# Kernel optimization log

Measured on AMD Instinct MI355X. Metric: run time of the kernel, lower is better.

The kernel has to match this reference:

```python
import jax, jax.numpy as jnp
import numpy as np

B, N, IN_DIM, DIM, HEADS = 2, 4096, 1024, 1024, 8
MAX_MASK = 2048
SCALE = DIM ** -0.5  # original uses full dim, not per-head dim


def setup_inputs() -> dict:
    key = jax.random.key(0)
    k_x, k_qkv, k_o, k_b, k_m = jax.random.split(key, 5)
    x = jax.random.normal(k_x, (B, N, IN_DIM), dtype=jnp.float32)
    W_qkv = jax.random.normal(k_qkv, (IN_DIM, 3 * DIM), dtype=jnp.float32) * 0.02
    W_out = jax.random.normal(k_o, (DIM, DIM), dtype=jnp.float32) * 0.02
    b_out = jax.random.normal(k_b, (DIM,), dtype=jnp.float32) * 0.02
    mask = jax.random.randint(k_m, (1, 1, MAX_MASK, MAX_MASK), 0, 2, dtype=jnp.int32)
    return {"x": x, "W_qkv": W_qkv, "W_out": W_out, "b_out": b_out,
            "mask": mask, "max_mask": MAX_MASK}


def reference(x, W_qkv, W_out, b_out, mask, max_mask):
    b, n, _ = x.shape
    d = DIM // HEADS
    qkv = x @ W_qkv                                   # [b, n, 3*dim]
    qkv = qkv.reshape(b, n, 3, HEADS, d).transpose(2, 0, 3, 1, 4)  # [3, b, h, n, d]
    q, k, v = qkv[0], qkv[1], qkv[2]
    dots = jnp.einsum('bhid,bhjd->bhij', q, k) * SCALE  # [b, h, n, n]
    # partial submatrix masking on the top-left [max_mask, max_mask] block
    m = max_mask
    sub = jnp.where(mask == 0, -jnp.inf, dots[:, :, :m, :m])
    dots = dots.at[:, :, :m, :m].set(sub)
    attn = jax.nn.softmax(dots, axis=-1)
    out = jnp.einsum('bhij,bhjd->bhid', attn, v)       # [b, h, n, d]
    out = out.transpose(0, 2, 1, 3).reshape(b, n, HEADS * d)
    return out @ W_out + b_out
```

## Files before the change

kernel.cpp:

```cpp
#include <hip/hip_runtime.h>
#include <hip/hip_bf16.h>
#include <stdint.h>


typedef __attribute__((ext_vector_type(8))) short short8;
typedef __attribute__((ext_vector_type(4))) float f32x4;

#define SCALE_Q 0.03125f

__device__ __forceinline__ unsigned short f2bf(float f) {
  union { float f; unsigned int u; } v;
  v.f = f;
  return (unsigned short)((v.u + 0x7fffu + ((v.u >> 16) & 1u)) >> 16);
}

__device__ __forceinline__ unsigned int pkbf2(float a, float b) {
  __hip_bfloat162 h = __float22bfloat162_rn(make_float2(a, b));
  union { __hip_bfloat162 h; unsigned int u; } c;
  c.h = h;
  return c.u;
}

__device__ __forceinline__ void gload_lds16(const void* g, void* l) {
  __builtin_amdgcn_global_load_lds(
      (const __attribute__((address_space(1))) uint32_t*)(uintptr_t)g,
      (__attribute__((address_space(3))) uint32_t*)(uintptr_t)l, 16, 0, 0);
}

__device__ __forceinline__ f32x4 zero4() {
  f32x4 z; z.x = 0.f; z.y = 0.f; z.z = 0.f; z.w = 0.f; return z;
}

__global__ __launch_bounds__(256) void k_cvt_x(const float* __restrict__ in,
                                               unsigned short* __restrict__ out) {
  const int t = blockIdx.x * 256 + threadIdx.x;
  const float4 v = ((const float4*)in)[t];
  ushort4 o;
  o.x = f2bf(v.x); o.y = f2bf(v.y); o.z = f2bf(v.z); o.w = f2bf(v.w);
  ((ushort4*)out)[t] = o;
}

__global__ __launch_bounds__(256) void k_cvt_wt(const float* __restrict__ w,
                                                unsigned short* __restrict__ wt,
                                                int Nn) {
  __shared__ float t[32][33];
  const int n0 = blockIdx.x << 5, k0 = blockIdx.y << 5;
  const int c = threadIdx.x & 31, r8 = threadIdx.x >> 5;
#pragma unroll
  for (int i = 0; i < 4; ++i) {
    const int r = (i << 3) + r8;
    t[r][c] = w[(long)(k0 + r) * Nn + n0 + c];
  }
  __syncthreads();
#pragma unroll
  for (int i = 0; i < 4; ++i) {
    const int r = (i << 3) + r8;
    wt[(long)(n0 + r) * 1024 + k0 + c] = f2bf(t[c][r]);
  }
}

__global__ __launch_bounds__(256, 2) void k_qkv_gemm(
    const unsigned short* __restrict__ A,
    const unsigned short* __restrict__ Bt,
    unsigned short* __restrict__ Qs, unsigned short* __restrict__ Ks,
    unsigned short* __restrict__ Vt) {
  __shared__ __align__(16) unsigned short lA[4][128][8];
  __shared__ __align__(16) unsigned short lB[4][128][8];
  const int tid = threadIdx.x;
  const int w = tid >> 6, ln = tid & 63;
  const int m15 = ln & 15, q4 = ln >> 4;
  const int wm = (w >> 1) << 6, wn = (w & 1) << 6;
  const int tn = blockIdx.x, tm = blockIdx.y;
  const int which = tn >> 3;
  const int h = tn & 7;

  f32x4 acc[4][4];
#pragma unroll
  for (int i = 0; i < 4; ++i)
#pragma unroll
    for (int j = 0; j < 4; ++j) acc[i][j] = zero4();

  if (which == 2) {
    for (int kb = 0; kb < 1024; kb += 32) {
      __syncthreads();
#pragma unroll
      for (int c = 0; c < 2; ++c) {
        const int p = ((c * 4 + w) << 10) + (ln << 4);
        const int g = p >> 11;
        const int r = (p & 2047) >> 4;
        gload_lds16(A + ((long)tm * 128 + r) * 1024 + kb + g * 8,
                    (char*)&lA[0][0][0] + p);
        gload_lds16(Bt + ((long)tn * 128 + r) * 1024 + kb + g * 8,
                    (char*)&lB[0][0][0] + p);
      }
      __syncthreads();
      short8 afr[4], bfr[4];
#pragma unroll
      for (int i = 0; i < 4; ++i)
        afr[i] = *(const short8*)&lA[q4][wm + i * 16 + m15][0];
#pragma unroll
      for (int j = 0; j < 4; ++j)
        bfr[j] = *(const short8*)&lB[q4][wn + j * 16 + m15][0];
#pragma unroll
      for (int i = 0; i < 4; ++i)
#pragma unroll
        for (int j = 0; j < 4; ++j)
          acc[i][j] = __builtin_amdgcn_mfma_f32_16x16x32_bf16(afr[i], bfr[j],
                                                              acc[i][j], 0, 0, 0);
    }
#pragma unroll
    for (int i = 0; i < 4; ++i) {
      const int m0 = (tm << 7) + wm + (i << 4) + (q4 << 2);
      const int b = m0 >> 12, row0 = m0 & 4095;
#pragma unroll
      for (int j = 0; j < 4; ++j) {
        const int dd = wn + (j << 4) + m15;
        const long bh = b * 8 + h;
        uint2 u;
        u.x = pkbf2(acc[i][j][0], acc[i][j][1]);
        u.y = pkbf2(acc[i][j][2], acc[i][j][3]);
        *(uint2*)&Vt[(bh * 128 + dd) * 4096 + row0] = u;
      }
    }
  } else {
    for (int kb = 0; kb < 1024; kb += 32) {
      __syncthreads();
#pragma unroll
      for (int c = 0; c < 2; ++c) {
        const int p = ((c * 4 + w) << 10) + (ln << 4);
        const int g = p >> 11;
        const int r = (p & 2047) >> 4;
        gload_lds16(A + ((long)tm * 128 + r) * 1024 + kb + g * 8,
                    (char*)&lA[0][0][0] + p);
        gload_lds16(Bt + ((long)tn * 128 + r) * 1024 + kb + g * 8,
                    (char*)&lB[0][0][0] + p);
      }
      __syncthreads();
      short8 afr[4], bfr[4];
#pragma unroll
      for (int i = 0; i < 4; ++i)
        afr[i] = *(const short8*)&lA[q4][wm + i * 16 + m15][0];
#pragma unroll
      for (int j = 0; j < 4; ++j)
        bfr[j] = *(const short8*)&lB[q4][wn + j * 16 + m15][0];
#pragma unroll
      for (int i = 0; i < 4; ++i)
#pragma unroll
        for (int j = 0; j < 4; ++j)
          acc[i][j] = __builtin_amdgcn_mfma_f32_16x16x32_bf16(bfr[j], afr[i],
                                                              acc[i][j], 0, 0, 0);
    }
    unsigned short* Dst = (which == 0) ? Qs : Ks;
    const float sc = (which == 0) ? SCALE_Q : 1.0f;
#pragma unroll
    for (int i = 0; i < 4; ++i) {
      const int m = (tm << 7) + wm + (i << 4) + m15;
      const int b = m >> 12, row = m & 4095;
      const long bh = b * 8 + h;
#pragma unroll
      for (int j = 0; j < 4; ++j) {
        const int dd0 = wn + (j << 4) + (q4 << 2);
        uint2 u;
        u.x = pkbf2(acc[i][j][0] * sc, acc[i][j][1] * sc);
        u.y = pkbf2(acc[i][j][2] * sc, acc[i][j][3] * sc);
        *(uint2*)&Dst[(bh * 4096 + row) * 128 + dd0] = u;
      }
    }
  }
}

__global__ __launch_bounds__(512, 2) void k_flash(
    const unsigned short* __restrict__ Qs, const unsigned short* __restrict__ Ks,
    const unsigned short* __restrict__ Vt, const int* __restrict__ mask,
    unsigned short* __restrict__ Ob) {
  __shared__ __align__(16) unsigned short lK[16][64][8];
  __shared__ __align__(16) unsigned short lV[8][128][8];
  __shared__ __align__(16) unsigned short lP[8][16][72];

  const int tid = threadIdx.x;
  const int w = tid >> 6, ln = tid & 63;
  const int m15 = ln & 15, q4 = ln >> 4;
  const int rowblk = blockIdx.x, bh = blockIdx.y;
  const int rbase = rowblk * 128 + w * 16;
  const int qrow = rbase + m15;

  const unsigned short* Qbh = Qs + (long)bh * 524288;
  const unsigned short* Kbh = Ks + (long)bh * 524288;
  const unsigned short* Vbh = Vt + (long)bh * 524288;

  short8 qf[4];
#pragma unroll
  for (int kk = 0; kk < 4; ++kk)
    qf[kk] = *(const short8*)(Qbh + (long)qrow * 128 + kk * 32 + q4 * 8);

  f32x4 o[8];
#pragma unroll
  for (int j = 0; j < 8; ++j) o[j] = zero4();
  f32x4 lacc = zero4();

  const bool maskblk = rowblk < 16;

  for (int kv = 0; kv < 4096; kv += 64) {
    __syncthreads();
#pragma unroll
    for (int c = 0; c < 2; ++c) {
      const int p = ((c * 8 + w) << 10) + (ln << 4);
      const int cs = p >> 10;
      const int j = (p & 1023) >> 4;
      gload_lds16(Kbh + (long)(kv + j) * 128 + cs * 8, (char*)&lK[0][0][0] + p);
    }
#pragma unroll
    for (int c = 0; c < 2; ++c) {
      const int p = ((c * 8 + w) << 10) + (ln << 4);
      const int cv = p >> 11;
      const int dv = (p & 2047) >> 4;
      gload_lds16(Vbh + (long)dv * 4096 + kv + cv * 8, (char*)&lV[0][0][0] + p);
    }
    __syncthreads();

    f32x4 s[4];
#pragma unroll
    for (int jt = 0; jt < 4; ++jt) s[jt] = zero4();
#pragma unroll
    for (int jt = 0; jt < 4; ++jt) {
#pragma unroll
      for (int kk = 0; kk < 4; ++kk) {
        const short8 kfr = *(const short8*)&lK[kk * 4 + q4][jt * 16 + m15][0];
        s[jt] = __builtin_amdgcn_mfma_f32_16x16x32_bf16(kfr, qf[kk], s[jt],
                                                        0, 0, 0);
      }
    }

    if (maskblk && kv < 2048) {
#pragma unroll
      for (int jt = 0; jt < 4; ++jt) {
        const int4 mv =
            *(const int4*)&mask[(long)qrow * 2048 + kv + jt * 16 + q4 * 4];
        s[jt].x = mv.x ? s[jt].x : -1e30f;
        s[jt].y = mv.y ? s[jt].y : -1e30f;
        s[jt].z = mv.z ? s[jt].z : -1e30f;
        s[jt].w = mv.w ? s[jt].w : -1e30f;
      }
    }

#pragma unroll
    for (int jt = 0; jt < 4; ++jt) {
      f32x4 p;
      p.x = __expf(s[jt].x); p.y = __expf(s[jt].y);
      p.z = __expf(s[jt].z); p.w = __expf(s[jt].w);
      lacc.x += p.x; lacc.y += p.y; lacc.z += p.z; lacc.w += p.w;
      uint2 u;
      u.x = pkbf2(p.x, p.y);
      u.y = pkbf2(p.z, p.w);
      *(uint2*)&lP[w][m15][jt * 16 + q4 * 4] = u;
    }
    __asm__ volatile("s_waitcnt lgkmcnt(0)" ::: "memory");

#pragma unroll
    for (int kk2 = 0; kk2 < 2; ++kk2) {
      const short8 pf = *(const short8*)&lP[w][m15][kk2 * 32 + q4 * 8];
#pragma unroll
      for (int jt2 = 0; jt2 < 8; ++jt2) {
        const short8 vf = *(const short8*)&lV[kk2 * 4 + q4][jt2 * 16 + m15][0];
        o[jt2] = __builtin_amdgcn_mfma_f32_16x16x32_bf16(pf, vf, o[jt2],
                                                         0, 0, 0);
      }
    }
  }

  float lh = lacc.x + lacc.y + lacc.z + lacc.w;
  lh += __shfl_xor(lh, 16);
  lh += __shfl_xor(lh, 32);
  const float linv = 1.0f / lh;
  float linv_r[4];
#pragma unroll
  for (int r = 0; r < 4; ++r) linv_r[r] = __shfl(linv, q4 * 4 + r);

  const int b = bh >> 3, h = bh & 7;
#pragma unroll
  for (int r = 0; r < 4; ++r) {
    const int row = rbase + q4 * 4 + r;
    unsigned short* op = Ob + ((long)(b * 4096 + row)) * 1024 + h * 128;
#pragma unroll
    for (int jt2 = 0; jt2 < 8; ++jt2)
      op[jt2 * 16 + m15] = f2bf(o[jt2][r] * linv_r[r]);
  }
}

__global__ __launch_bounds__(256, 2) void k_proj_gemm(
    const unsigned short* __restrict__ A,
    const unsigned short* __restrict__ Bt,
    const float* __restrict__ bias, float* __restrict__ Out) {
  __shared__ __align__(16) unsigned short lA[4][128][8];
  __shared__ __align__(16) unsigned short lB[4][128][8];
  const int tid = threadIdx.x;
  const int w = tid >> 6, ln = tid & 63;
  const int m15 = ln & 15, q4 = ln >> 4;
  const int wm = (w >> 1) << 6, wn = (w & 1) << 6;
  const int tn = blockIdx.x, tm = blockIdx.y;

  f32x4 acc[4][4];
#pragma unroll
  for (int i = 0; i < 4; ++i)
#pragma unroll
    for (int j = 0; j < 4; ++j) acc[i][j] = zero4();

  for (int kb = 0; kb < 1024; kb += 32) {
    __syncthreads();
#pragma unroll
    for (int c = 0; c < 2; ++c) {
      const int p = ((c * 4 + w) << 10) + (ln << 4);
      const int g = p >> 11;
      const int r = (p & 2047) >> 4;
      gload_lds16(A + ((long)tm * 128 + r) * 1024 + kb + g * 8,
                  (char*)&lA[0][0][0] + p);
      gload_lds16(Bt + ((long)tn * 128 + r) * 1024 + kb + g * 8,
                  (char*)&lB[0][0][0] + p);
    }
    __syncthreads();
    short8 afr[4], bfr[4];
#pragma unroll
    for (int i = 0; i < 4; ++i)
      afr[i] = *(const short8*)&lA[q4][wm + i * 16 + m15][0];
#pragma unroll
    for (int j = 0; j < 4; ++j)
      bfr[j] = *(const short8*)&lB[q4][wn + j * 16 + m15][0];
#pragma unroll
    for (int i = 0; i < 4; ++i)
#pragma unroll
      for (int j = 0; j < 4; ++j)
        acc[i][j] = __builtin_amdgcn_mfma_f32_16x16x32_bf16(afr[i], bfr[j],
                                                            acc[i][j], 0, 0, 0);
  }

#pragma unroll
  for (int i = 0; i < 4; ++i)
#pragma unroll
    for (int r = 0; r < 4; ++r) {
      const int m = (tm << 7) + wm + (i << 4) + (q4 << 2) + r;
#pragma unroll
      for (int j = 0; j < 4; ++j) {
        const int n = (tn << 7) + wn + (j << 4) + m15;
        Out[(long)m * 1024 + n] = acc[i][j][r] + bias[n];
      }
    }
}

extern "C" void kernel_launch(void* const* d_in, const int* in_sizes, int n_in,
                              void* d_out, int out_size, void* d_ws,
                              size_t ws_size, hipStream_t stream) {
  const float* x = (const float*)d_in[0];
  const float* Wqkv = (const float*)d_in[1];
  const float* Wout = (const float*)d_in[2];
  const float* bout = (const float*)d_in[3];
  const int* mask = (const int*)d_in[4];
  float* out = (float*)d_out;

  char* ws = (char*)d_ws;
  unsigned short* xb     = (unsigned short*)(ws);
  unsigned short* wqkv_t = (unsigned short*)(ws + 16777216);
  unsigned short* wout_t = (unsigned short*)(ws + 23068672);
  unsigned short* Qs     = (unsigned short*)(ws + 25165824);
  unsigned short* Ks     = (unsigned short*)(ws + 41943040);
  unsigned short* Vt     = (unsigned short*)(ws + 58720256);
  unsigned short* Ob     = xb;

  hipLaunchKernelGGL(k_cvt_x, dim3(8192), dim3(256), 0, stream, x, xb);
  hipLaunchKernelGGL(k_cvt_wt, dim3(96, 32), dim3(256), 0, stream, Wqkv, wqkv_t, 3072);
  hipLaunchKernelGGL(k_cvt_wt, dim3(32, 32), dim3(256), 0, stream, Wout, wout_t, 1024);
  hipLaunchKernelGGL(k_qkv_gemm, dim3(24, 64), dim3(256), 0, stream,
                     xb, wqkv_t, Qs, Ks, Vt);
  hipLaunchKernelGGL(k_flash, dim3(32, 16), dim3(512), 0, stream,
                     Qs, Ks, Vt, mask, Ob);
  hipLaunchKernelGGL(k_proj_gemm, dim3(8, 64), dim3(256), 0, stream,
                     Ob, wout_t, bout, out);
}
```

Baseline: 470.9 us.

## Double-buffer K/V in flash kernel, process two query groups per wave, bitpack mask

The flash kernel now has each wave handle 32 query rows in two groups that share every K and V fragment loaded from LDS. The grid shrinks to half as many row blocks. K/V tiles are double-buffered so the next tile loads while the current one computes, which drops one barrier per iteration, and s_setprio hints are placed around the MFMA sections. A new kernel packs the int32 mask into 64-bit ballot words in the now-free wqkv_t workspace, which cuts mask read traffic inside the attention loop. The trade-offs are higher register and LDS use, which may lower occupancy, fewer blocks in flight, and one extra kernel launch.

```diff
diff --git a/kernel.cpp b/kernel.cpp
--- a/kernel.cpp
+++ b/kernel.cpp
@@ -57,6 +57,13 @@
     const int r = (i << 3) + r8;
     wt[(long)(n0 + r) * 1024 + k0 + c] = f2bf(t[c][r]);
   }
+}
+
+__global__ __launch_bounds__(256) void k_mask_bits(
+    const int* __restrict__ m, unsigned long long* __restrict__ mb) {
+  const int t = blockIdx.x * 256 + threadIdx.x;
+  const unsigned long long b = __ballot(m[t] != 0);
+  if ((threadIdx.x & 63) == 0) mb[t >> 6] = b;
 }
 
 __global__ __launch_bounds__(256, 2) void k_qkv_gemm(
@@ -171,119 +178,164 @@
 
 __global__ __launch_bounds__(512, 2) void k_flash(
     const unsigned short* __restrict__ Qs, const unsigned short* __restrict__ Ks,
-    const unsigned short* __restrict__ Vt, const int* __restrict__ mask,
+    const unsigned short* __restrict__ Vt,
+    const unsigned long long* __restrict__ mbits,
     unsigned short* __restrict__ Ob) {
-  __shared__ __align__(16) unsigned short lK[16][64][8];
-  __shared__ __align__(16) unsigned short lV[8][128][8];
-  __shared__ __align__(16) unsigned short lP[8][16][72];
+  __shared__ __align__(16) unsigned short lK[2][16][64][8];
+  __shared__ __align__(16) unsigned short lV[2][8][128][8];
+  __shared__ __align__(16) unsigned short lP[8][2][16][72];
 
   const int tid = threadIdx.x;
   const int w = tid >> 6, ln = tid & 63;
   const int m15 = ln & 15, q4 = ln >> 4;
   const int rowblk = blockIdx.x, bh = blockIdx.y;
-  const int rbase = rowblk * 128 + w * 16;
-  const int qrow = rbase + m15;
+  const int rbase = rowblk * 256 + w * 32;
+  const int rq0 = rbase + m15;
+  const int rq1 = rbase + 16 + m15;
 
   const unsigned short* Qbh = Qs + (long)bh * 524288;
   const unsigned short* Kbh = Ks + (long)bh * 524288;
   const unsigned short* Vbh = Vt + (long)bh * 524288;
 
-  short8 qf[4];
-#pragma unroll
-  for (int kk = 0; kk < 4; ++kk)
-    qf[kk] = *(const short8*)(Qbh + (long)qrow * 128 + kk * 32 + q4 * 8);
-
-  f32x4 o[8];
-#pragma unroll
-  for (int j = 0; j < 8; ++j) o[j] = zero4();
-  f32x4 lacc = zero4();
-
-  const bool maskblk = rowblk < 16;
-
+  short8 qf[2][4];
+#pragma unroll
+  for (int kk = 0; kk < 4; ++kk) {
+    qf[0][kk] = *(const short8*)(Qbh + (long)rq0 * 128 + kk * 32 + q4 * 8);
+    qf[1][kk] = *(const short8*)(Qbh + (long)rq1 * 128 + kk * 32 + q4 * 8);
+  }
+
+  f32x4 o[2][8];
+#pragma unroll
+  for (int qg = 0; qg < 2; ++qg)
+#pragma unroll
+    for (int j = 0; j < 8; ++j) o[qg][j] = zero4();
+  f32x4 lacc[2];
+  lacc[0] = zero4(); lacc[1] = zero4();
+
+  const bool maskblk = rowblk < 8;
+
+#define STAGE_KV(dst, kvoff)                                              \
+  {                                                                       \
+    _Pragma("unroll")                                                     \
+    for (int c = 0; c < 2; ++c) {                                         \
+      const int p = ((c * 8 + w) << 10) + (ln << 4);                      \
+      const int cs = p >> 10;                                             \
+      const int j = (p & 1023) >> 4;                                      \
+      gload_lds16(Kbh + (long)((kvoff) + j) * 128 + cs * 8,               \
+                  (char*)&lK[dst][0][0][0] + p);                          \
+    }                                                                     \
+    _Pragma("unroll")                                                     \
+    for (int c = 0; c < 2; ++c) {                                         \
+      const int p = ((c * 8 + w) << 10) + (ln << 4);                      \
+      const int cv = p >> 11;                                             \
+      const int dv = (p & 2047) >> 4;                                     \
+      gload_lds16(Vbh + (long)dv * 4096 + (kvoff) + cv * 8,               \
+                  (char*)&lV[dst][0][0][0] + p);                          \
+    }                                                                     \
+  }
+
+  STAGE_KV(0, 0);
+  __syncthreads();
+
+  int cur = 0;
   for (int kv = 0; kv < 4096; kv += 64) {
+    unsigned long long mw0 = 0ull, mw1 = 0ull;
+    const bool domask = maskblk && (kv < 2048);
+    if (domask) {
+      mw0 = mbits[(long)rq0 * 32 + (kv >> 6)];
+      mw1 = mbits[(long)rq1 * 32 + (kv >> 6)];
+    }
+
+    const int nb = cur ^ 1;
+    if (kv + 64 < 4096) STAGE_KV(nb, kv + 64);
+
+    f32x4 s[2][4];
+#pragma unroll
+    for (int jt = 0; jt < 4; ++jt) { s[0][jt] = zero4(); s[1][jt] = zero4(); }
+    __builtin_amdgcn_s_setprio(1);
+#pragma unroll
+    for (int jt = 0; jt < 4; ++jt) {
+#pragma unroll
+      for (int kk = 0; kk < 4; ++kk) {
+        const short8 kfr = *(const short8*)&lK[cur][kk * 4 + q4][jt * 16 + m15][0];
+        s[0][jt] = __builtin_amdgcn_mfma_f32_16x16x32_bf16(kfr, qf[0][kk],
+                                                           s[0][jt], 0, 0, 0);
+        s[1][jt] = __builtin_amdgcn_mfma_f32_16x16x32_bf16(kfr, qf[1][kk],
+                                                           s[1][jt], 0, 0, 0);
+      }
+    }
+    __builtin_amdgcn_s_setprio(0);
+
+    if (domask) {
+#pragma unroll
+      for (int jt = 0; jt < 4; ++jt) {
+        const unsigned int u0 =
+            (jt & 2) ? (unsigned int)(mw0 >> 32) : (unsigned int)mw0;
+        const unsigned int u1 =
+            (jt & 2) ? (unsigned int)(mw1 >> 32) : (unsigned int)mw1;
+        const int base = ((jt & 1) << 4) + (q4 << 2);
+#pragma unroll
+        for (int r = 0; r < 4; ++r) {
+          if (!((u0 >> (base + r)) & 1u)) s[0][jt][r] = -1e30f;
+          if (!((u1 >> (base + r)) & 1u)) s[1][jt][r] = -1e30f;
+        }
+      }
+    }
+
+#pragma unroll
+    for (int jt = 0; jt < 4; ++jt) {
+      f32x4 p0, p1;
+      p0.x = __expf(s[0][jt].x); p0.y = __expf(s[0][jt].y);
+      p0.z = __expf(s[0][jt].z); p0.w = __expf(s[0][jt].w);
+      p1.x = __expf(s[1][jt].x); p1.y = __expf(s[1][jt].y);
+      p1.z = __expf(s[1][jt].z); p1.w = __expf(s[1][jt].w);
+      lacc[0] += p0; lacc[1] += p1;
+      uint2 u0, u1;
+      u0.x = pkbf2(p0.x, p0.y); u0.y = pkbf2(p0.z, p0.w);
+      u1.x = pkbf2(p1.x, p1.y); u1.y = pkbf2(p1.z, p1.w);
+      *(uint2*)&lP[w][0][m15][jt * 16 + q4 * 4] = u0;
+      *(uint2*)&lP[w][1][m15][jt * 16 + q4 * 4] = u1;
+    }
+    __asm__ volatile("s_waitcnt lgkmcnt(0)" ::: "memory");
+    __builtin_amdgcn_sched_barrier(0);
+
+    __builtin_amdgcn_s_setprio(1);
+#pragma unroll
+    for (int kk2 = 0; kk2 < 2; ++kk2) {
+      const short8 pf0 = *(const short8*)&lP[w][0][m15][kk2 * 32 + q4 * 8];
+      const short8 pf1 = *(const short8*)&lP[w][1][m15][kk2 * 32 + q4 * 8];
+#pragma unroll
+      for (int jt2 = 0; jt2 < 8; ++jt2) {
+        const short8 vf = *(const short8*)&lV[cur][kk2 * 4 + q4][jt2 * 16 + m15][0];
+        o[0][jt2] = __builtin_amdgcn_mfma_f32_16x16x32_bf16(pf0, vf,
+                                                            o[0][jt2], 0, 0, 0);
+        o[1][jt2] = __builtin_amdgcn_mfma_f32_16x16x32_bf16(pf1, vf,
+                                                            o[1][jt2], 0, 0, 0);
+      }
+    }
+    __builtin_amdgcn_s_setprio(0);
+
     __syncthreads();
-#pragma unroll
-    for (int c = 0; c < 2; ++c) {
-      const int p = ((c * 8 + w) << 10) + (ln << 4);
-      const int cs = p >> 10;
-      const int j = (p & 1023) >> 4;
-      gload_lds16(Kbh + (long)(kv + j) * 128 + cs * 8, (char*)&lK[0][0][0] + p);
-    }
-#pragma unroll
-    for (int c = 0; c < 2; ++c) {
-      const int p = ((c * 8 + w) << 10) + (ln << 4);
-      const int cv = p >> 11;
-      const int dv = (p & 2047) >> 4;
-      gload_lds16(Vbh + (long)dv * 4096 + kv + cv * 8, (char*)&lV[0][0][0] + p);
-    }
-    __syncthreads();
-
-    f32x4 s[4];
-#pragma unroll
-    for (int jt = 0; jt < 4; ++jt) s[jt] = zero4();
-#pragma unroll
-    for (int jt = 0; jt < 4; ++jt) {
-#pragma unroll
-      for (int kk = 0; kk < 4; ++kk) {
-        const short8 kfr = *(const short8*)&lK[kk * 4 + q4][jt * 16 + m15][0];
-        s[jt] = __builtin_amdgcn_mfma_f32_16x16x32_bf16(kfr, qf[kk], s[jt],
-                                                        0, 0, 0);
-      }
-    }
-
-    if (maskblk && kv < 2048) {
-#pragma unroll
-      for (int jt = 0; jt < 4; ++jt) {
-        const int4 mv =
-            *(const int4*)&mask[(long)qrow * 2048 + kv + jt * 16 + q4 * 4];
-        s[jt].x = mv.x ? s[jt].x : -1e30f;
-        s[jt].y = mv.y ? s[jt].y : -1e30f;
-        s[jt].z = mv.z ? s[jt].z : -1e30f;
-        s[jt].w = mv.w ? s[jt].w : -1e30f;
-      }
-    }
-
-#pragma unroll
-    for (int jt = 0; jt < 4; ++jt) {
-      f32x4 p;
-      p.x = __expf(s[jt].x); p.y = __expf(s[jt].y);
-      p.z = __expf(s[jt].z); p.w = __expf(s[jt].w);
-      lacc.x += p.x; lacc.y += p.y; lacc.z += p.z; lacc.w += p.w;
-      uint2 u;
-      u.x = pkbf2(p.x, p.y);
-      u.y = pkbf2(p.z, p.w);
-      *(uint2*)&lP[w][m15][jt * 16 + q4 * 4] = u;
-    }
-    __asm__ volatile("s_waitcnt lgkmcnt(0)" ::: "memory");
-
-#pragma unroll
-    for (int kk2 = 0; kk2 < 2; ++kk2) {
-      const short8 pf = *(const short8*)&lP[w][m15][kk2 * 32 + q4 * 8];
-#pragma unroll
-      for (int jt2 = 0; jt2 < 8; ++jt2) {
-        const short8 vf = *(const short8*)&lV[kk2 * 4 + q4][jt2 * 16 + m15][0];
-        o[jt2] = __builtin_amdgcn_mfma_f32_16x16x32_bf16(pf, vf, o[jt2],
-                                                         0, 0, 0);
-      }
-    }
-  }
-
-  float lh = lacc.x + lacc.y + lacc.z + lacc.w;
-  lh += __shfl_xor(lh, 16);
-  lh += __shfl_xor(lh, 32);
-  const float linv = 1.0f / lh;
-  float linv_r[4];
-#pragma unroll
-  for (int r = 0; r < 4; ++r) linv_r[r] = __shfl(linv, q4 * 4 + r);
+    cur = nb;
+  }
+#undef STAGE_KV
 
   const int b = bh >> 3, h = bh & 7;
 #pragma unroll
-  for (int r = 0; r < 4; ++r) {
-    const int row = rbase + q4 * 4 + r;
-    unsigned short* op = Ob + ((long)(b * 4096 + row)) * 1024 + h * 128;
-#pragma unroll
-    for (int jt2 = 0; jt2 < 8; ++jt2)
-      op[jt2 * 16 + m15] = f2bf(o[jt2][r] * linv_r[r]);
+  for (int qg = 0; qg < 2; ++qg) {
+    float lh = lacc[qg].x + lacc[qg].y + lacc[qg].z + lacc[qg].w;
+    lh += __shfl_xor(lh, 16);
+    lh += __shfl_xor(lh, 32);
+    const float linv = 1.0f / lh;
+#pragma unroll
+    for (int r = 0; r < 4; ++r) {
+      const float li = __shfl(linv, q4 * 4 + r);
+      const int row = rbase + qg * 16 + q4 * 4 + r;
+      unsigned short* op = Ob + ((long)(b * 4096 + row)) * 1024 + h * 128;
+#pragma unroll
+      for (int jt2 = 0; jt2 < 8; ++jt2)
+        op[jt2 * 16 + m15] = f2bf(o[qg][jt2][r] * li);
+    }
   }
 }
 
@@ -364,14 +416,17 @@
   unsigned short* Ks     = (unsigned short*)(ws + 41943040);
   unsigned short* Vt     = (unsigned short*)(ws + 58720256);
   unsigned short* Ob     = xb;
+  unsigned long long* mbits = (unsigned long long*)wqkv_t;
 
   hipLaunchKernelGGL(k_cvt_x, dim3(8192), dim3(256), 0, stream, x, xb);
   hipLaunchKernelGGL(k_cvt_wt, dim3(96, 32), dim3(256), 0, stream, Wqkv, wqkv_t, 3072);
   hipLaunchKernelGGL(k_cvt_wt, dim3(32, 32), dim3(256), 0, stream, Wout, wout_t, 1024);
   hipLaunchKernelGGL(k_qkv_gemm, dim3(24, 64), dim3(256), 0, stream,
                      xb, wqkv_t, Qs, Ks, Vt);
-  hipLaunchKernelGGL(k_flash, dim3(32, 16), dim3(512), 0, stream,
-                     Qs, Ks, Vt, mask, Ob);
+  hipLaunchKernelGGL(k_mask_bits, dim3(16384), dim3(256), 0, stream,
+                     mask, mbits);
+  hipLaunchKernelGGL(k_flash, dim3(16, 16), dim3(512), 0, stream,
+                     Qs, Ks, Vt, mbits, Ob);
   hipLaunchKernelGGL(k_proj_gemm, dim3(8, 64), dim3(256), 0, stream,
                      Ob, wout_t, bout, out);
 }
```

Measured after the change: 436.5 us. 1.08x faster.
